# Performance work log

Hardware: AMD Instinct MI355X
Metric: run time of the kernel (lower is better)

## Reference

```python
import jax, jax.numpy as jnp
import numpy as np

N = 100000   # nodes
E = 3200000  # directed edges
F_IN = 128   # data.num_node_features
H = 16       # hidden
C = 2        # output classes (hard-coded in module)


def _glorot(key, fan_in, fan_out):
    s = jnp.sqrt(6.0 / (fan_in + fan_out)).astype(jnp.float32)
    return jax.random.uniform(key, (fan_in, fan_out), jnp.float32, -s, s)


def setup_inputs() -> dict:
    key = jax.random.key(0)
    ks = jax.random.split(key, 5)
    x = jax.random.normal(ks[0], (N, F_IN), jnp.float32)
    edge_index = jax.random.randint(ks[1], (2, E), 0, N, dtype=jnp.int64)
    return {
        "x": x,
        "edge_index": edge_index,
        "W1": _glorot(ks[2], F_IN, H), "b1": jnp.zeros((H,), jnp.float32),
        "W2": _glorot(ks[3], H, H),    "b2": jnp.zeros((H,), jnp.float32),
        "W3": _glorot(ks[4], H, C),    "b3": jnp.zeros((C,), jnp.float32),
    }


def _gcn_conv(x, W, b, src, dst, norm, n):
    # PyG GCNConv: linear transform, then normalized gather -> scatter-add, + bias
    h = x @ W                                   # [N, out]
    msg = h[src] * norm[:, None]                # [E+N, out] gather over source nodes
    out = jax.ops.segment_sum(msg, dst, num_segments=n)  # scatter-add at targets
    return out + b


def reference(x, edge_index, W1, b1, W2, b2, W3, b3):
    n = x.shape[0]
    loop = jnp.arange(n, dtype=edge_index.dtype)
    src = jnp.concatenate([edge_index[0], loop])  # add self-loops (PyG default)
    dst = jnp.concatenate([edge_index[1], loop])
    # symmetric normalization: deg^{-1/2}[src] * deg^{-1/2}[dst], deg = in-degree w/ self-loops
    deg = jax.ops.segment_sum(jnp.ones(src.shape, jnp.float32), dst, num_segments=n)
    dis = jnp.where(deg > 0, jax.lax.rsqrt(jnp.maximum(deg, 1.0)), 0.0)
    norm = dis[src] * dis[dst]
    # dropout is identity in eval mode
    h = jax.nn.relu(_gcn_conv(x, W1, b1, src, dst, norm, n))
    h = jax.nn.relu(_gcn_conv(h, W2, b2, src, dst, norm, n))
    h = _gcn_conv(h, W3, b3, src, dst, norm, n)
    return jax.nn.log_softmax(h, axis=1)
```

## Files before the change

kernel.cpp:

```cpp
#include <hip/hip_runtime.h>
#include <math.h>

#define NSB   512
#define BSH   8
#define BKN   256
#define ESMAX 6272
#define SLOT  10240

typedef _Float16 h8  __attribute__((ext_vector_type(8)));
typedef _Float16 h4  __attribute__((ext_vector_type(4)));
typedef _Float16 h2v __attribute__((ext_vector_type(2)));

__device__ inline int wave_scan_incl(int v) {
    int lane = threadIdx.x & 63;
#pragma unroll
    for (int d = 1; d < 64; d <<= 1) {
        int t = __shfl_up(v, d, 64);
        if (lane >= d) v += t;
    }
    return v;
}


__global__ void k_bucket(const int* __restrict__ src, const int* __restrict__ dst,
                         int* __restrict__ gcur, unsigned* __restrict__ col,
                         int e, int nbuck, int es) {
    __shared__ unsigned sorted[ESMAX];
    __shared__ unsigned char sbuck[ESMAX];
    __shared__ int lc[512], lofE[512], lcur[512], soff[512];
    __shared__ int wsum[8];
    int tid = threadIdx.x;
    lc[tid] = 0;
    __syncthreads();
    int lo = blockIdx.x * es;
    int hi = min(lo + es, e);
    for (int i = lo + tid; i < hi; i += 512)
        atomicAdd(&lc[dst[i] >> BSH], 1);
    __syncthreads();
    int c = lc[tid];
    int inc = wave_scan_incl(c);
    int wid = tid >> 6;
    if ((tid & 63) == 63) wsum[wid] = inc;
    __syncthreads();
    int wofs = 0;
#pragma unroll
    for (int w = 0; w < 8; w++) wofs += (w < wid) ? wsum[w] : 0;
    int excl = inc - c + wofs;
    lofE[tid] = excl;
    lcur[tid] = excl;
    if (tid < nbuck && c > 0)
        soff[tid] = tid * SLOT + atomicAdd(&gcur[tid], c);
    __syncthreads();
    for (int i = lo + tid; i < hi; i += 512) {
        int d = dst[i];
        int b = d >> BSH;
        int p = atomicAdd(&lcur[b], 1);
        sorted[p] = ((unsigned)src[i] << BSH) | (unsigned)(d & (BKN - 1));
        sbuck[p] = (unsigned char)(b & 255);
    }
    __syncthreads();
    int cnt_ = hi - lo;
    int split = (nbuck > 256) ? lofE[256] : 0x7fffffff;
    for (int i = tid; i < cnt_; i += 512) {
        int b = sbuck[i] | ((i >= split) ? 256 : 0);
        col[soff[b] + (i - lofE[b])] = sorted[i];
    }
}


__global__ void k_sort(const unsigned* __restrict__ col, const int* __restrict__ gcur,
                       int* __restrict__ col2, int* __restrict__ rs,
                       int* __restrict__ re, float* __restrict__ dis,
                       int n, int nbuck) {
    __shared__ int cnt[BKN];
    __shared__ int cur[BKN];
    __shared__ int wsum[4];
    int tid = threadIdx.x;
    int b = blockIdx.x;
    int lo = b * SLOT;
    int hi = lo + gcur[b];
    if (tid < BKN) cnt[tid] = 0;
    __syncthreads();
    for (int i = lo + tid; i < hi; i += 512)
        atomicAdd(&cnt[col[i] & (BKN - 1u)], 1);
    __syncthreads();
    int c = (tid < BKN) ? cnt[tid] : 0;
    int inc = wave_scan_incl(c);
    int wid = tid >> 6;
    if (tid < BKN && (tid & 63) == 63) wsum[wid] = inc;
    __syncthreads();
    if (tid < BKN) {
        int wofs = 0;
#pragma unroll
        for (int w = 0; w < 4; w++) wofs += (w < wid) ? wsum[w] : 0;
        int excl = inc - c + wofs;
        cur[tid] = lo + excl;
        int node = (b << BSH) + tid;
        if (node < n) {
            rs[node] = lo + excl;
            re[node] = lo + excl + c;
            dis[node] = rsqrtf((float)(c + 1));
        }
    }
    __syncthreads();
    for (int i = lo + tid; i < hi; i += 512) {
        unsigned v = col[i];
        int pos = atomicAdd(&cur[v & (BKN - 1u)], 1);
        col2[pos] = (int)(v >> BSH);
    }
}


__global__ __launch_bounds__(512) void k_linear1s(
        const float* __restrict__ x, const float* __restrict__ W,
        const float* __restrict__ dis, _Float16* __restrict__ hs, int n) {
    __shared__ float sW[2048];
    int tid = threadIdx.x;
    for (int i = tid; i < 2048; i += 512) sW[i] = W[i];
    __syncthreads();
    int cg = tid & 3;
    int kg = (tid >> 2) & 7;
    int nl = tid >> 5;
    float wr[16][4];
#pragma unroll
    for (int j = 0; j < 16; j++)
#pragma unroll
        for (int cc = 0; cc < 4; cc++)
            wr[j][cc] = sW[(kg * 16 + j) * 16 + cg * 4 + cc];
    int nodeBase = blockIdx.x * 128 + nl;
    for (int it = 0; it < 8; it++) {
        int node = nodeBase + it * 16;
        float a0 = 0.f, a1 = 0.f, a2 = 0.f, a3 = 0.f;
        if (node < n) {
            const float4* xr = (const float4*)(x + (size_t)node * 128 + kg * 16);
#pragma unroll
            for (int j4 = 0; j4 < 4; j4++) {
                float4 xv = xr[j4];
                float xs0 = xv.x, xs1 = xv.y, xs2 = xv.z, xs3 = xv.w;
                int j = j4 * 4;
                a0 += xs0 * wr[j][0] + xs1 * wr[j+1][0] + xs2 * wr[j+2][0] + xs3 * wr[j+3][0];
                a1 += xs0 * wr[j][1] + xs1 * wr[j+1][1] + xs2 * wr[j+2][1] + xs3 * wr[j+3][1];
                a2 += xs0 * wr[j][2] + xs1 * wr[j+1][2] + xs2 * wr[j+2][2] + xs3 * wr[j+3][2];
                a3 += xs0 * wr[j][3] + xs1 * wr[j+1][3] + xs2 * wr[j+2][3] + xs3 * wr[j+3][3];
            }
        }
#pragma unroll
        for (int m = 4; m <= 16; m <<= 1) {
            a0 += __shfl_xor(a0, m);
            a1 += __shfl_xor(a1, m);
            a2 += __shfl_xor(a2, m);
            a3 += __shfl_xor(a3, m);
        }
        if (kg == 0 && node < n) {
            float d = dis[node];
            h4 o;
            o[0] = (_Float16)(a0 * d);
            o[1] = (_Float16)(a1 * d);
            o[2] = (_Float16)(a2 * d);
            o[3] = (_Float16)(a3 * d);
            *((h4*)(hs + (size_t)node * 16 + cg * 4)) = o;
        }
    }
}


__global__ void k_pullA(const _Float16* __restrict__ hs, const int* __restrict__ rs,
                        const int* __restrict__ re, const int* __restrict__ col2,
                        const float* __restrict__ dis, const float* __restrict__ bb,
                        const float* __restrict__ W, _Float16* __restrict__ hsOut, int n) {
    __shared__ float sW[256];
    __shared__ float sb[16];
    if (threadIdx.x < 256) sW[threadIdx.x] = W[threadIdx.x];
    if (threadIdx.x < 16) sb[threadIdx.x] = bb[threadIdx.x];
    __syncthreads();
    long long t = (long long)blockIdx.x * blockDim.x + threadIdx.x;
    int node = (int)(t >> 3), sub = (int)(t & 7);
    int q = sub & 1, qt = sub >> 1;
    if (node >= n) return;
    const h8* H = (const h8*)hs;
    float acc[8];
    if (qt == 0) {
        h8 self = H[(size_t)node * 2 + q];
#pragma unroll
        for (int j = 0; j < 8; j++) acc[j] = (float)self[j];
    } else {
#pragma unroll
        for (int j = 0; j < 8; j++) acc[j] = 0.f;
    }
    int b = rs[node], e2 = re[node];
    int i = b + qt;
    for (; i + 12 < e2; i += 16) {
        int s0 = col2[i], s1 = col2[i + 4], s2 = col2[i + 8], s3 = col2[i + 12];
        h8 v0 = H[(size_t)s0 * 2 + q];
        h8 v1 = H[(size_t)s1 * 2 + q];
        h8 v2 = H[(size_t)s2 * 2 + q];
        h8 v3 = H[(size_t)s3 * 2 + q];
#pragma unroll
        for (int j = 0; j < 8; j++)
            acc[j] += (float)v0[j] + (float)v1[j] + (float)v2[j] + (float)v3[j];
    }
    for (; i < e2; i += 4) {
        h8 v = H[(size_t)col2[i] * 2 + q];
#pragma unroll
        for (int j = 0; j < 8; j++) acc[j] += (float)v[j];
    }
#pragma unroll
    for (int j = 0; j < 8; j++) {
        acc[j] += __shfl_xor(acc[j], 2);
        acc[j] += __shfl_xor(acc[j], 4);
    }
    float d = dis[node];
    float va[16];
#pragma unroll
    for (int j = 0; j < 8; j++) {
        int k = q * 8 + j;
        float v = acc[j] * d + sb[k];
        v = v > 0.f ? v : 0.f;
        float other = __shfl_xor(v, 1);
        va[j]     = q ? other : v;
        va[8 + j] = q ? v : other;
    }
    if (qt == 0) {
        h8 o;
#pragma unroll
        for (int j = 0; j < 8; j++) {
            int c = q * 8 + j;
            float s = 0.f;
#pragma unroll
            for (int k = 0; k < 16; k++) s += va[k] * sW[k * 16 + c];
            o[j] = (_Float16)(s * d);
        }
        ((h8*)hsOut)[(size_t)node * 2 + q] = o;
    }
}


__global__ void k_pullB(const _Float16* __restrict__ hs, const int* __restrict__ rs,
                        const int* __restrict__ re, const int* __restrict__ col2,
                        const float* __restrict__ dis, const float* __restrict__ bb,
                        const float* __restrict__ W, _Float16* __restrict__ hs2, int n) {
    __shared__ float sW[32];
    __shared__ float sb[16];
    if (threadIdx.x < 32) sW[threadIdx.x] = W[threadIdx.x];
    if (threadIdx.x < 16) sb[threadIdx.x] = bb[threadIdx.x];
    __syncthreads();
    long long t = (long long)blockIdx.x * blockDim.x + threadIdx.x;
    int node = (int)(t >> 3), sub = (int)(t & 7);
    int q = sub & 1, qt = sub >> 1;
    if (node >= n) return;
    const h8* H = (const h8*)hs;
    float acc[8];
    if (qt == 0) {
        h8 self = H[(size_t)node * 2 + q];
#pragma unroll
        for (int j = 0; j < 8; j++) acc[j] = (float)self[j];
    } else {
#pragma unroll
        for (int j = 0; j < 8; j++) acc[j] = 0.f;
    }
    int b = rs[node], e2 = re[node];
    int i = b + qt;
    for (; i + 12 < e2; i += 16) {
        int s0 = col2[i], s1 = col2[i + 4], s2 = col2[i + 8], s3 = col2[i + 12];
        h8 v0 = H[(size_t)s0 * 2 + q];
        h8 v1 = H[(size_t)s1 * 2 + q];
        h8 v2 = H[(size_t)s2 * 2 + q];
        h8 v3 = H[(size_t)s3 * 2 + q];
#pragma unroll
        for (int j = 0; j < 8; j++)
            acc[j] += (float)v0[j] + (float)v1[j] + (float)v2[j] + (float)v3[j];
    }
    for (; i < e2; i += 4) {
        h8 v = H[(size_t)col2[i] * 2 + q];
#pragma unroll
        for (int j = 0; j < 8; j++) acc[j] += (float)v[j];
    }
#pragma unroll
    for (int j = 0; j < 8; j++) {
        acc[j] += __shfl_xor(acc[j], 2);
        acc[j] += __shfl_xor(acc[j], 4);
    }
    float d = dis[node];
    float p0 = 0.f, p1 = 0.f;
#pragma unroll
    for (int j = 0; j < 8; j++) {
        int k = q * 8 + j;
        float v = acc[j] * d + sb[k];
        v = v > 0.f ? v : 0.f;
        p0 += v * sW[k * 2 + 0];
        p1 += v * sW[k * 2 + 1];
    }
    p0 += __shfl_xor(p0, 1);
    p1 += __shfl_xor(p1, 1);
    if (sub == 0) {
        h2v o;
        o[0] = (_Float16)(p0 * d);
        o[1] = (_Float16)(p1 * d);
        ((h2v*)hs2)[node] = o;
    }
}


__global__ void k_pull2lsm(const _Float16* __restrict__ hs2, const int* __restrict__ rs,
                           const int* __restrict__ re, const int* __restrict__ col2,
                           const float* __restrict__ dis, const float* __restrict__ b3,
                           float* __restrict__ out, int n) {
    long long t = (long long)blockIdx.x * blockDim.x + threadIdx.x;
    int node = (int)(t >> 2), qt = (int)(t & 3);
    if (node >= n) return;
    const h2v* H = (const h2v*)hs2;
    float a0 = 0.f, a1 = 0.f;
    if (qt == 0) {
        h2v self = H[node];
        a0 = (float)self[0]; a1 = (float)self[1];
    }
    int b = rs[node], e2 = re[node];
    int i = b + qt;
    for (; i + 12 < e2; i += 16) {
        h2v v0 = H[col2[i]];
        h2v v1 = H[col2[i + 4]];
        h2v v2 = H[col2[i + 8]];
        h2v v3 = H[col2[i + 12]];
        a0 += (float)v0[0] + (float)v1[0] + (float)v2[0] + (float)v3[0];
        a1 += (float)v0[1] + (float)v1[1] + (float)v2[1] + (float)v3[1];
    }
    for (; i < e2; i += 4) {
        h2v v = H[col2[i]];
        a0 += (float)v[0];
        a1 += (float)v[1];
    }
    a0 += __shfl_xor(a0, 1); a0 += __shfl_xor(a0, 2);
    a1 += __shfl_xor(a1, 1); a1 += __shfl_xor(a1, 2);
    if (qt == 0) {
        float d = dis[node];
        float z0 = a0 * d + b3[0];
        float z1 = a1 * d + b3[1];
        float m = fmaxf(z0, z1);
        float l = m + logf(expf(z0 - m) + expf(z1 - m));
        float2 o = {z0 - l, z1 - l};
        ((float2*)out)[node] = o;
    }
}


extern "C" void kernel_launch(void* const* d_in, const int* in_sizes, int n_in,
                              void* d_out, int out_size, void* d_ws, size_t ws_size,
                              hipStream_t stream) {
    const float* x  = (const float*)d_in[0];
    const int*   ei = (const int*)d_in[1];
    const float* W1 = (const float*)d_in[2];
    const float* b1 = (const float*)d_in[3];
    const float* W2 = (const float*)d_in[4];
    const float* b2 = (const float*)d_in[5];
    const float* W3 = (const float*)d_in[6];
    const float* b3 = (const float*)d_in[7];
    float* out = (float*)d_out;

    const int N = in_sizes[0] / 128;
    const int E = in_sizes[1] / 2;
    const int* src = ei;
    const int* dst = ei + E;

    const int NBUCK = (N + BKN - 1) >> BSH;
    const int ES = (E + NSB - 1) / NSB;

    char* ws = (char*)d_ws;
    size_t off = 0;
    auto alloc = [&](size_t bytes) {
        void* p = ws + off;
        off += (bytes + 255) & ~(size_t)255;
        return p;
    };
    int*       gcur = (int*)alloc((size_t)NBUCK * sizeof(int));
    unsigned*  col  = (unsigned*)alloc((size_t)NBUCK * SLOT * sizeof(unsigned));
    int*       col2 = (int*)alloc((size_t)NBUCK * SLOT * sizeof(int));
    int*       rs   = (int*)alloc((size_t)N * sizeof(int));
    int*       re   = (int*)alloc((size_t)N * sizeof(int));
    float*     dis  = (float*)alloc((size_t)N * sizeof(float));
    _Float16*  hsA  = (_Float16*)alloc((size_t)N * 16 * sizeof(_Float16));
    _Float16*  hsB  = (_Float16*)alloc((size_t)N * 16 * sizeof(_Float16));
    _Float16*  hs2  = (_Float16*)alloc((size_t)N * 2 * sizeof(_Float16));

    const int B = 256;
    auto g = [&](long long work) { return (int)((work + B - 1) / B); };

    hipMemsetAsync(gcur, 0, (size_t)NBUCK * sizeof(int), stream);
    k_bucket<<<NSB, 512, 0, stream>>>(src, dst, gcur, col, E, NBUCK, ES);
    k_sort<<<NBUCK, 512, 0, stream>>>(col, gcur, col2, rs, re, dis, N, NBUCK);

    k_linear1s<<<(N + 127) / 128, 512, 0, stream>>>(x, W1, dis, hsA, N);

    k_pullA<<<g((long long)N * 8), B, 0, stream>>>(hsA, rs, re, col2, dis, b1, W2, hsB, N);

    k_pullB<<<g((long long)N * 8), B, 0, stream>>>(hsB, rs, re, col2, dis, b2, W3, hs2, N);

    k_pull2lsm<<<g((long long)N * 4), B, 0, stream>>>(hs2, rs, re, col2, dis, b3, out, N);
}
```

Baseline: 244.3 us.

## Use 4 lanes per node in hidden pulls and stage sorted columns in LDS

The two 16-wide aggregation kernels now assign four threads per node, each gathering the full 32-byte row per edge, instead of eight threads split across half-rows. The 16x16 transform is divided across the four lanes by output column, and the cross-lane shuffle for the ReLU vector is removed. Separately, k_sort scatters into a shared-memory buffer and then writes col2 contiguously, replacing scattered global stores with coalesced ones. Each thread now holds more registers, and halving the thread count may lower memory-level parallelism.

```diff
diff --git a/kernel.cpp b/kernel.cpp
--- a/kernel.cpp
+++ b/kernel.cpp
@@ -68,17 +68,20 @@
 }
 
 
-__global__ void k_sort(const unsigned* __restrict__ col, const int* __restrict__ gcur,
-                       int* __restrict__ col2, int* __restrict__ rs,
-                       int* __restrict__ re, float* __restrict__ dis,
-                       int n, int nbuck) {
+__global__ __launch_bounds__(512) void k_sort(
+        const unsigned* __restrict__ col, const int* __restrict__ gcur,
+        int* __restrict__ col2, int* __restrict__ rs,
+        int* __restrict__ re, float* __restrict__ dis,
+        int n, int nbuck) {
     __shared__ int cnt[BKN];
     __shared__ int cur[BKN];
     __shared__ int wsum[4];
+    __shared__ int sdat[SLOT];
     int tid = threadIdx.x;
     int b = blockIdx.x;
     int lo = b * SLOT;
-    int hi = lo + gcur[b];
+    int tot = gcur[b];
+    int hi = lo + tot;
     if (tid < BKN) cnt[tid] = 0;
     __syncthreads();
     for (int i = lo + tid; i < hi; i += 512)
@@ -94,7 +97,7 @@
 #pragma unroll
         for (int w = 0; w < 4; w++) wofs += (w < wid) ? wsum[w] : 0;
         int excl = inc - c + wofs;
-        cur[tid] = lo + excl;
+        cur[tid] = excl;
         int node = (b << BSH) + tid;
         if (node < n) {
             rs[node] = lo + excl;
@@ -106,8 +109,11 @@
     for (int i = lo + tid; i < hi; i += 512) {
         unsigned v = col[i];
         int pos = atomicAdd(&cur[v & (BKN - 1u)], 1);
-        col2[pos] = (int)(v >> BSH);
-    }
+        sdat[pos] = (int)(v >> BSH);
+    }
+    __syncthreads();
+    for (int i = tid; i < tot; i += 512)
+        col2[lo + i] = sdat[i];
 }
 
 
@@ -164,135 +170,134 @@
 }
 
 
-__global__ void k_pullA(const _Float16* __restrict__ hs, const int* __restrict__ rs,
-                        const int* __restrict__ re, const int* __restrict__ col2,
-                        const float* __restrict__ dis, const float* __restrict__ bb,
-                        const float* __restrict__ W, _Float16* __restrict__ hsOut, int n) {
+__global__ __launch_bounds__(256) void k_pullA(
+        const _Float16* __restrict__ hs, const int* __restrict__ rs,
+        const int* __restrict__ re, const int* __restrict__ col2,
+        const float* __restrict__ dis, const float* __restrict__ bb,
+        const float* __restrict__ W, _Float16* __restrict__ hsOut, int n) {
     __shared__ float sW[256];
     __shared__ float sb[16];
     if (threadIdx.x < 256) sW[threadIdx.x] = W[threadIdx.x];
     if (threadIdx.x < 16) sb[threadIdx.x] = bb[threadIdx.x];
     __syncthreads();
     long long t = (long long)blockIdx.x * blockDim.x + threadIdx.x;
-    int node = (int)(t >> 3), sub = (int)(t & 7);
-    int q = sub & 1, qt = sub >> 1;
+    int node = (int)(t >> 2), qt = (int)(t & 3);
     if (node >= n) return;
     const h8* H = (const h8*)hs;
-    float acc[8];
+    float acc[16];
     if (qt == 0) {
-        h8 self = H[(size_t)node * 2 + q];
-#pragma unroll
-        for (int j = 0; j < 8; j++) acc[j] = (float)self[j];
+        h8 s0 = H[(size_t)node * 2];
+        h8 s1 = H[(size_t)node * 2 + 1];
+#pragma unroll
+        for (int j = 0; j < 8; j++) { acc[j] = (float)s0[j]; acc[8 + j] = (float)s1[j]; }
     } else {
 #pragma unroll
-        for (int j = 0; j < 8; j++) acc[j] = 0.f;
+        for (int j = 0; j < 16; j++) acc[j] = 0.f;
     }
     int b = rs[node], e2 = re[node];
     int i = b + qt;
     for (; i + 12 < e2; i += 16) {
         int s0 = col2[i], s1 = col2[i + 4], s2 = col2[i + 8], s3 = col2[i + 12];
-        h8 v0 = H[(size_t)s0 * 2 + q];
-        h8 v1 = H[(size_t)s1 * 2 + q];
-        h8 v2 = H[(size_t)s2 * 2 + q];
-        h8 v3 = H[(size_t)s3 * 2 + q];
-#pragma unroll
-        for (int j = 0; j < 8; j++)
-            acc[j] += (float)v0[j] + (float)v1[j] + (float)v2[j] + (float)v3[j];
+        h8 a0 = H[(size_t)s0 * 2], b0 = H[(size_t)s0 * 2 + 1];
+        h8 a1 = H[(size_t)s1 * 2], b1 = H[(size_t)s1 * 2 + 1];
+        h8 a2 = H[(size_t)s2 * 2], b2 = H[(size_t)s2 * 2 + 1];
+        h8 a3 = H[(size_t)s3 * 2], b3 = H[(size_t)s3 * 2 + 1];
+#pragma unroll
+        for (int j = 0; j < 8; j++) {
+            acc[j]     += (float)a0[j] + (float)a1[j] + (float)a2[j] + (float)a3[j];
+            acc[8 + j] += (float)b0[j] + (float)b1[j] + (float)b2[j] + (float)b3[j];
+        }
     }
     for (; i < e2; i += 4) {
-        h8 v = H[(size_t)col2[i] * 2 + q];
-#pragma unroll
-        for (int j = 0; j < 8; j++) acc[j] += (float)v[j];
-    }
-#pragma unroll
-    for (int j = 0; j < 8; j++) {
+        int s = col2[i];
+        h8 a = H[(size_t)s * 2], bq = H[(size_t)s * 2 + 1];
+#pragma unroll
+        for (int j = 0; j < 8; j++) { acc[j] += (float)a[j]; acc[8 + j] += (float)bq[j]; }
+    }
+#pragma unroll
+    for (int j = 0; j < 16; j++) {
+        acc[j] += __shfl_xor(acc[j], 1);
         acc[j] += __shfl_xor(acc[j], 2);
-        acc[j] += __shfl_xor(acc[j], 4);
     }
     float d = dis[node];
     float va[16];
 #pragma unroll
-    for (int j = 0; j < 8; j++) {
-        int k = q * 8 + j;
-        float v = acc[j] * d + sb[k];
-        v = v > 0.f ? v : 0.f;
-        float other = __shfl_xor(v, 1);
-        va[j]     = q ? other : v;
-        va[8 + j] = q ? v : other;
-    }
-    if (qt == 0) {
-        h8 o;
-#pragma unroll
-        for (int j = 0; j < 8; j++) {
-            int c = q * 8 + j;
-            float s = 0.f;
-#pragma unroll
-            for (int k = 0; k < 16; k++) s += va[k] * sW[k * 16 + c];
-            o[j] = (_Float16)(s * d);
-        }
-        ((h8*)hsOut)[(size_t)node * 2 + q] = o;
-    }
-}
-
-
-__global__ void k_pullB(const _Float16* __restrict__ hs, const int* __restrict__ rs,
-                        const int* __restrict__ re, const int* __restrict__ col2,
-                        const float* __restrict__ dis, const float* __restrict__ bb,
-                        const float* __restrict__ W, _Float16* __restrict__ hs2, int n) {
+    for (int k = 0; k < 16; k++) {
+        float v = acc[k] * d + sb[k];
+        va[k] = v > 0.f ? v : 0.f;
+    }
+    h4 o;
+#pragma unroll
+    for (int cc = 0; cc < 4; cc++) {
+        int cidx = (qt << 2) + cc;
+        float s = 0.f;
+#pragma unroll
+        for (int k = 0; k < 16; k++) s += va[k] * sW[k * 16 + cidx];
+        o[cc] = (_Float16)(s * d);
+    }
+    *((h4*)(hsOut + (size_t)node * 16 + (qt << 2))) = o;
+}
+
+
+__global__ __launch_bounds__(256) void k_pullB(
+        const _Float16* __restrict__ hs, const int* __restrict__ rs,
+        const int* __restrict__ re, const int* __restrict__ col2,
+        const float* __restrict__ dis, const float* __restrict__ bb,
+        const float* __restrict__ W, _Float16* __restrict__ hs2, int n) {
     __shared__ float sW[32];
     __shared__ float sb[16];
     if (threadIdx.x < 32) sW[threadIdx.x] = W[threadIdx.x];
     if (threadIdx.x < 16) sb[threadIdx.x] = bb[threadIdx.x];
     __syncthreads();
     long long t = (long long)blockIdx.x * blockDim.x + threadIdx.x;
-    int node = (int)(t >> 3), sub = (int)(t & 7);
-    int q = sub & 1, qt = sub >> 1;
+    int node = (int)(t >> 2), qt = (int)(t & 3);
     if (node >= n) return;
     const h8* H = (const h8*)hs;
-    float acc[8];
+    float acc[16];
     if (qt == 0) {
-        h8 self = H[(size_t)node * 2 + q];
-#pragma unroll
-        for (int j = 0; j < 8; j++) acc[j] = (float)self[j];
+        h8 s0 = H[(size_t)node * 2];
+        h8 s1 = H[(size_t)node * 2 + 1];
+#pragma unroll
+        for (int j = 0; j < 8; j++) { acc[j] = (float)s0[j]; acc[8 + j] = (float)s1[j]; }
     } else {
 #pragma unroll
-        for (int j = 0; j < 8; j++) acc[j] = 0.f;
+        for (int j = 0; j < 16; j++) acc[j] = 0.f;
     }
     int b = rs[node], e2 = re[node];
     int i = b + qt;
     for (; i + 12 < e2; i += 16) {
         int s0 = col2[i], s1 = col2[i + 4], s2 = col2[i + 8], s3 = col2[i + 12];
-        h8 v0 = H[(size_t)s0 * 2 + q];
-        h8 v1 = H[(size_t)s1 * 2 + q];
-        h8 v2 = H[(size_t)s2 * 2 + q];
-        h8 v3 = H[(size_t)s3 * 2 + q];
-#pragma unroll
-        for (int j = 0; j < 8; j++)
-            acc[j] += (float)v0[j] + (float)v1[j] + (float)v2[j] + (float)v3[j];
+        h8 a0 = H[(size_t)s0 * 2], b0 = H[(size_t)s0 * 2 + 1];
+        h8 a1 = H[(size_t)s1 * 2], b1 = H[(size_t)s1 * 2 + 1];
+        h8 a2 = H[(size_t)s2 * 2], b2 = H[(size_t)s2 * 2 + 1];
+        h8 a3 = H[(size_t)s3 * 2], b3 = H[(size_t)s3 * 2 + 1];
+#pragma unroll
+        for (int j = 0; j < 8; j++) {
+            acc[j]     += (float)a0[j] + (float)a1[j] + (float)a2[j] + (float)a3[j];
+            acc[8 + j] += (float)b0[j] + (float)b1[j] + (float)b2[j] + (float)b3[j];
+        }
     }
     for (; i < e2; i += 4) {
-        h8 v = H[(size_t)col2[i] * 2 + q];
-#pragma unroll
-        for (int j = 0; j < 8; j++) acc[j] += (float)v[j];
-    }
-#pragma unroll
-    for (int j = 0; j < 8; j++) {
+        int s = col2[i];
+        h8 a = H[(size_t)s * 2], bq = H[(size_t)s * 2 + 1];
+#pragma unroll
+        for (int j = 0; j < 8; j++) { acc[j] += (float)a[j]; acc[8 + j] += (float)bq[j]; }
+    }
+#pragma unroll
+    for (int j = 0; j < 16; j++) {
+        acc[j] += __shfl_xor(acc[j], 1);
         acc[j] += __shfl_xor(acc[j], 2);
-        acc[j] += __shfl_xor(acc[j], 4);
     }
     float d = dis[node];
     float p0 = 0.f, p1 = 0.f;
 #pragma unroll
-    for (int j = 0; j < 8; j++) {
-        int k = q * 8 + j;
-        float v = acc[j] * d + sb[k];
+    for (int k = 0; k < 16; k++) {
+        float v = acc[k] * d + sb[k];
         v = v > 0.f ? v : 0.f;
         p0 += v * sW[k * 2 + 0];
         p1 += v * sW[k * 2 + 1];
     }
-    p0 += __shfl_xor(p0, 1);
-    p1 += __shfl_xor(p1, 1);
-    if (sub == 0) {
+    if (qt == 0) {
         h2v o;
         o[0] = (_Float16)(p0 * d);
         o[1] = (_Float16)(p1 * d);
@@ -301,10 +306,11 @@
 }
 
 
-__global__ void k_pull2lsm(const _Float16* __restrict__ hs2, const int* __restrict__ rs,
-                           const int* __restrict__ re, const int* __restrict__ col2,
-                           const float* __restrict__ dis, const float* __restrict__ b3,
-                           float* __restrict__ out, int n) {
+__global__ __launch_bounds__(256) void k_pull2lsm(
+        const _Float16* __restrict__ hs2, const int* __restrict__ rs,
+        const int* __restrict__ re, const int* __restrict__ col2,
+        const float* __restrict__ dis, const float* __restrict__ b3,
+        float* __restrict__ out, int n) {
     long long t = (long long)blockIdx.x * blockDim.x + threadIdx.x;
     int node = (int)(t >> 2), qt = (int)(t & 3);
     if (node >= n) return;
@@ -390,9 +396,9 @@
 
     k_linear1s<<<(N + 127) / 128, 512, 0, stream>>>(x, W1, dis, hsA, N);
 
-    k_pullA<<<g((long long)N * 8), B, 0, stream>>>(hsA, rs, re, col2, dis, b1, W2, hsB, N);
-
-    k_pullB<<<g((long long)N * 8), B, 0, stream>>>(hsB, rs, re, col2, dis, b2, W3, hs2, N);
+    k_pullA<<<g((long long)N * 4), B, 0, stream>>>(hsA, rs, re, col2, dis, b1, W2, hsB, N);
+
+    k_pullB<<<g((long long)N * 4), B, 0, stream>>>(hsB, rs, re, col2, dis, b2, W3, hs2, N);
 
     k_pull2lsm<<<g((long long)N * 4), B, 0, stream>>>(hs2, rs, re, col2, dis, b3, out, N);
 }
```

Result: no change. 247.8 us (+1.4%).

## Replace global-atomic bucket scatter with per-chunk count/offset tables and LDS gather

Applied to the files above, without the earlier changes.

The bucketing pass no longer reserves space through global atomics and scatters edges into per-bucket slots. Each chunk now writes its locally sorted edges contiguously, plus a per-bucket count and offset table. The sort kernel prefix-scans those counts across chunks, gathers each bucket's segments into shared memory, and does the counting sort from there. This removes the memset, the global atomics and the scattered writes, but the gather becomes per-thread serial loops over small strided segments, and the kernel now needs a large shared-memory buffer that may lower occupancy.

```diff
diff --git a/kernel.cpp b/kernel.cpp
--- a/kernel.cpp
+++ b/kernel.cpp
@@ -2,6 +2,7 @@
 #include <math.h>
 
 #define NSB   512
+#define CB    512
 #define BSH   8
 #define BKN   256
 #define ESMAX 6272
@@ -22,91 +23,108 @@
 }
 
 
-__global__ void k_bucket(const int* __restrict__ src, const int* __restrict__ dst,
-                         int* __restrict__ gcur, unsigned* __restrict__ col,
-                         int e, int nbuck, int es) {
+__global__ __launch_bounds__(512) void k_bucket(
+        const int* __restrict__ src, const int* __restrict__ dst,
+        unsigned* __restrict__ col, int* __restrict__ cnt2d, int* __restrict__ ofs2d,
+        int e, int es) {
     __shared__ unsigned sorted[ESMAX];
-    __shared__ unsigned char sbuck[ESMAX];
-    __shared__ int lc[512], lofE[512], lcur[512], soff[512];
+    __shared__ int lc[512], lcur[512];
     __shared__ int wsum[8];
     int tid = threadIdx.x;
+    int c = blockIdx.x;
     lc[tid] = 0;
     __syncthreads();
-    int lo = blockIdx.x * es;
+    int lo = c * es;
     int hi = min(lo + es, e);
     for (int i = lo + tid; i < hi; i += 512)
         atomicAdd(&lc[dst[i] >> BSH], 1);
     __syncthreads();
-    int c = lc[tid];
-    int inc = wave_scan_incl(c);
+    int cv = lc[tid];
+    int inc = wave_scan_incl(cv);
     int wid = tid >> 6;
     if ((tid & 63) == 63) wsum[wid] = inc;
     __syncthreads();
     int wofs = 0;
 #pragma unroll
     for (int w = 0; w < 8; w++) wofs += (w < wid) ? wsum[w] : 0;
-    int excl = inc - c + wofs;
-    lofE[tid] = excl;
+    int excl = inc - cv + wofs;
     lcur[tid] = excl;
-    if (tid < nbuck && c > 0)
-        soff[tid] = tid * SLOT + atomicAdd(&gcur[tid], c);
+    cnt2d[(size_t)c * CB + tid] = cv;
+    ofs2d[(size_t)c * CB + tid] = excl;
     __syncthreads();
     for (int i = lo + tid; i < hi; i += 512) {
         int d = dst[i];
         int b = d >> BSH;
         int p = atomicAdd(&lcur[b], 1);
         sorted[p] = ((unsigned)src[i] << BSH) | (unsigned)(d & (BKN - 1));
-        sbuck[p] = (unsigned char)(b & 255);
     }
     __syncthreads();
     int cnt_ = hi - lo;
-    int split = (nbuck > 256) ? lofE[256] : 0x7fffffff;
-    for (int i = tid; i < cnt_; i += 512) {
-        int b = sbuck[i] | ((i >= split) ? 256 : 0);
-        col[soff[b] + (i - lofE[b])] = sorted[i];
-    }
-}
-
-
-__global__ void k_sort(const unsigned* __restrict__ col, const int* __restrict__ gcur,
-                       int* __restrict__ col2, int* __restrict__ rs,
-                       int* __restrict__ re, float* __restrict__ dis,
-                       int n, int nbuck) {
-    __shared__ int cnt[BKN];
-    __shared__ int cur[BKN];
-    __shared__ int wsum[4];
+    for (int i = tid; i < cnt_; i += 512)
+        col[(size_t)c * es + i] = sorted[i];
+}
+
+
+__global__ __launch_bounds__(512) void k_sort(
+        const unsigned* __restrict__ col, const int* __restrict__ cnt2d,
+        const int* __restrict__ ofs2d,
+        int* __restrict__ col2, int* __restrict__ rs,
+        int* __restrict__ re, float* __restrict__ dis,
+        int n, int nch, int es) {
+    __shared__ int sdat[SLOT];
+    __shared__ int cnt[BKN], cur[BKN];
+    __shared__ int wsum8[8];
+    __shared__ int wsum4[4];
     int tid = threadIdx.x;
     int b = blockIdx.x;
     int lo = b * SLOT;
-    int hi = lo + gcur[b];
+
+    int nc = (tid < nch) ? cnt2d[(size_t)tid * CB + b] : 0;
+    int inc = wave_scan_incl(nc);
+    int wid = tid >> 6;
+    if ((tid & 63) == 63) wsum8[wid] = inc;
+    __syncthreads();
+    int wofs = 0, tot = 0;
+#pragma unroll
+    for (int w = 0; w < 8; w++) {
+        wofs += (w < wid) ? wsum8[w] : 0;
+        tot += wsum8[w];
+    }
+    int base = inc - nc + wofs;
+    if (tot > SLOT) tot = SLOT;
+    if (base + nc > SLOT) nc = max(0, SLOT - base);
     if (tid < BKN) cnt[tid] = 0;
-    __syncthreads();
-    for (int i = lo + tid; i < hi; i += 512)
-        atomicAdd(&cnt[col[i] & (BKN - 1u)], 1);
+    if (nc > 0) {
+        size_t sbase = (size_t)tid * es + ofs2d[(size_t)tid * CB + b];
+        for (int k = 0; k < nc; k++)
+            sdat[base + k] = (int)col[sbase + k];
+    }
+    __syncthreads();
+    for (int i = tid; i < tot; i += 512)
+        atomicAdd(&cnt[sdat[i] & (BKN - 1)], 1);
     __syncthreads();
     int c = (tid < BKN) ? cnt[tid] : 0;
-    int inc = wave_scan_incl(c);
-    int wid = tid >> 6;
-    if (tid < BKN && (tid & 63) == 63) wsum[wid] = inc;
+    int inc2 = wave_scan_incl(c);
+    if (tid < BKN && (tid & 63) == 63) wsum4[wid] = inc2;
     __syncthreads();
     if (tid < BKN) {
-        int wofs = 0;
-#pragma unroll
-        for (int w = 0; w < 4; w++) wofs += (w < wid) ? wsum[w] : 0;
-        int excl = inc - c + wofs;
-        cur[tid] = lo + excl;
+        int wofs2 = 0;
+#pragma unroll
+        for (int w = 0; w < 4; w++) wofs2 += (w < wid) ? wsum4[w] : 0;
+        int excl2 = inc2 - c + wofs2;
+        cur[tid] = lo + excl2;
         int node = (b << BSH) + tid;
         if (node < n) {
-            rs[node] = lo + excl;
-            re[node] = lo + excl + c;
+            rs[node] = lo + excl2;
+            re[node] = lo + excl2 + c;
             dis[node] = rsqrtf((float)(c + 1));
         }
     }
     __syncthreads();
-    for (int i = lo + tid; i < hi; i += 512) {
-        unsigned v = col[i];
-        int pos = atomicAdd(&cur[v & (BKN - 1u)], 1);
-        col2[pos] = (int)(v >> BSH);
+    for (int i = tid; i < tot; i += 512) {
+        int v = sdat[i];
+        int pos = atomicAdd(&cur[v & (BKN - 1)], 1);
+        col2[pos] = v >> BSH;
     }
 }
 
@@ -371,22 +389,23 @@
         off += (bytes + 255) & ~(size_t)255;
         return p;
     };
-    int*       gcur = (int*)alloc((size_t)NBUCK * sizeof(int));
-    unsigned*  col  = (unsigned*)alloc((size_t)NBUCK * SLOT * sizeof(unsigned));
-    int*       col2 = (int*)alloc((size_t)NBUCK * SLOT * sizeof(int));
-    int*       rs   = (int*)alloc((size_t)N * sizeof(int));
-    int*       re   = (int*)alloc((size_t)N * sizeof(int));
-    float*     dis  = (float*)alloc((size_t)N * sizeof(float));
-    _Float16*  hsA  = (_Float16*)alloc((size_t)N * 16 * sizeof(_Float16));
-    _Float16*  hsB  = (_Float16*)alloc((size_t)N * 16 * sizeof(_Float16));
-    _Float16*  hs2  = (_Float16*)alloc((size_t)N * 2 * sizeof(_Float16));
+    unsigned*  col   = (unsigned*)alloc((size_t)NSB * ES * sizeof(unsigned));
+    int*       cnt2d = (int*)alloc((size_t)NSB * CB * sizeof(int));
+    int*       ofs2d = (int*)alloc((size_t)NSB * CB * sizeof(int));
+    int*       col2  = (int*)alloc((size_t)NBUCK * SLOT * sizeof(int));
+    int*       rs    = (int*)alloc((size_t)N * sizeof(int));
+    int*       re    = (int*)alloc((size_t)N * sizeof(int));
+    float*     dis   = (float*)alloc((size_t)N * sizeof(float));
+    _Float16*  hsA   = (_Float16*)alloc((size_t)N * 16 * sizeof(_Float16));
+    _Float16*  hsB   = (_Float16*)alloc((size_t)N * 16 * sizeof(_Float16));
+    _Float16*  hs2   = (_Float16*)alloc((size_t)N * 2 * sizeof(_Float16));
 
     const int B = 256;
     auto g = [&](long long work) { return (int)((work + B - 1) / B); };
 
-    hipMemsetAsync(gcur, 0, (size_t)NBUCK * sizeof(int), stream);
-    k_bucket<<<NSB, 512, 0, stream>>>(src, dst, gcur, col, E, NBUCK, ES);
-    k_sort<<<NBUCK, 512, 0, stream>>>(col, gcur, col2, rs, re, dis, N, NBUCK);
+    k_bucket<<<NSB, 512, 0, stream>>>(src, dst, col, cnt2d, ofs2d, E, ES);
+
+    k_sort<<<NBUCK, 512, 0, stream>>>(col, cnt2d, ofs2d, col2, rs, re, dis, N, NSB, ES);
 
     k_linear1s<<<(N + 127) / 128, 512, 0, stream>>>(x, W1, dis, hsA, N);
 
```

New measurement: 237.0 us. -3.0%, faster.
